# Kernel tuning notes

Hardware: AMD Instinct MI355X
Metric: run time of the kernel (lower is better)

The kernel has to match this reference:

```python
import jax, jax.numpy as jnp
from jax import lax
import numpy as np

W = 64          # net_width
NITER = 10
THRESH = 1e-3
MSTEP = 1.0


def setup_inputs() -> dict:
    key = jax.random.key(0)
    ks = jax.random.split(key, 10)
    B, Nh, DIM = 8, 16384, 1024
    eye = jnp.eye(W, dtype=jnp.float32)
    return {
        'y_re': jax.random.normal(ks[0], (B, 1, Nh), jnp.float32),
        'y_im': jax.random.normal(ks[1], (B, 1, Nh), jnp.float32),
        'H_re': jax.random.normal(ks[2], (32768, DIM), jnp.float32) / np.sqrt(DIM),
        'H_im': jax.random.normal(ks[3], (32768, DIM), jnp.float32) / np.sqrt(DIM),
        # torch inits: estep.weight=I, estep.bias=0, update.weight=I, memory.weight=1e-6*I;
        # add small perturbations so the math is non-degenerate.
        'estep_w': eye + 0.05 * jax.random.normal(ks[4], (W, W), jnp.float32),
        'estep_b': jnp.zeros((W,), jnp.float32),
        'update_w': eye + 0.05 * jax.random.normal(ks[5], (W, W), jnp.float32),
        'update_b': 0.02 * jax.random.normal(ks[6], (W,), jnp.float32),
        'memory_w': 1e-6 * eye + 0.01 * jax.random.normal(ks[7], (W, W), jnp.float32),
        'memory_b': 0.02 * jax.random.normal(ks[8], (W,), jnp.float32),
    }


def _forward(y_re, y_im, H_re, H_im, estep_w, estep_b, update_w, update_b, memory_w, memory_b):
    y = (y_re + 1j * y_im).astype(jnp.complex64)          # [B,1,Nh]
    y = jnp.concatenate([y, jnp.conj(y)], axis=2)         # [B,1,N]
    H = (H_re + 1j * H_im).astype(jnp.complex64)          # [N,DIM]
    B, N = y.shape[0], y.shape[2]
    DIM = H.shape[1]
    nb = N // W
    Hb = H.reshape(nb, W, DIM)                            # [nb,W,DIM]
    yb = y.reshape(B, nb, W).transpose(1, 0, 2)[:, :, None, :]  # [nb,B,1,W]

    x0 = jnp.zeros((B, 1, DIM), jnp.complex64)
    tau0 = jnp.ones((nb, B, 1, W), jnp.float32)

    def block_step(xk, blk):
        H_i, y_i, tau_i = blk                              # [W,DIM], [B,1,W], [B,1,W]
        zk = jnp.einsum('bod,wd->bow', xk, H_i)            # [B,1,W] complex
        r = y_i - zk
        a2 = jnp.abs(r) ** 2                               # [B,1,W] float32
        # expectation_step: xt / std(xt) (torch.std = unbiased, global)
        xt = a2 / jnp.std(a2, ddof=1)
        ht = jax.nn.sigmoid(xt @ estep_w.T + estep_b)
        tau_new = jax.nn.relu(ht @ update_w.T + update_b + tau_i @ memory_w.T + memory_b)
        sigma2 = jnp.mean(a2, axis=2, keepdims=True)       # [B,1,1]
        residual = MSTEP * r * tau_new / sigma2            # complex
        xk = xk + jnp.einsum('bow,wd->bod', residual, jnp.conj(H_i)) / (W * DIM)
        return xk, tau_new

    def iteration(carry, _):
        xk, tau = carry
        xk, tau_new = lax.scan(block_step, xk, (Hb, yb, tau))  # sequential over blocks
        # soft threshold: sgn(x) * relu(|x| - threshold * max|x|)
        ax = jnp.abs(xk)
        m = jnp.max(ax)
        sgn = jnp.where(ax > 0, xk / jnp.where(ax > 0, ax, 1.0), 0.0 + 0.0j)
        xk = sgn * jax.nn.relu(ax - THRESH * m)
        return (xk, tau_new), None

    (xk, tau), _ = lax.scan(iteration, (x0, tau0), None, length=NITER)
    tau_out = tau[:, :, 0, :].transpose(1, 0, 2)           # [B,nb,W]
    return jnp.real(xk), tau_out


def reference(y_re, y_im, H_re, H_im, estep_w, estep_b, update_w, update_b, memory_w, memory_b):
    return _forward(y_re, y_im, H_re, H_im, estep_w, estep_b,
                    update_w, update_b, memory_w, memory_b)
```

## Files before the change

### kernel.cpp

```cpp
#include <hip/hip_runtime.h>
#include <hip/hip_cooperative_groups.h>
#include <math.h>

namespace cg = cooperative_groups;

#define NT  256
#define NWG 64
#define SCOPE_AG __HIP_MEMORY_SCOPE_AGENT

__device__ __forceinline__ float ld_f(const float* p) {
    return __hip_atomic_load(p, __ATOMIC_RELAXED, SCOPE_AG);
}
__device__ __forceinline__ void st_f(float* p, float v) {
    __hip_atomic_store(p, v, __ATOMIC_RELAXED, SCOPE_AG);
}
__device__ __forceinline__ unsigned ld_u(const unsigned* p) {
    return __hip_atomic_load(p, __ATOMIC_RELAXED, SCOPE_AG);
}
__device__ __forceinline__ void st_u(unsigned* p, unsigned v) {
    __hip_atomic_store(p, v, __ATOMIC_RELAXED, SCOPE_AG);
}
__device__ __forceinline__ float2 ld_f2(const float2* p) {
    unsigned long long u = __hip_atomic_load((const unsigned long long*)p, __ATOMIC_RELAXED, SCOPE_AG);
    float2 r;
    r.x = __uint_as_float((unsigned)u);
    r.y = __uint_as_float((unsigned)(u >> 32));
    return r;
}
__device__ __forceinline__ void st_f2(float2* p, float2 v) {
    unsigned long long u = ((unsigned long long)__float_as_uint(v.y) << 32) | (unsigned long long)__float_as_uint(v.x);
    __hip_atomic_store((unsigned long long*)p, u, __ATOMIC_RELAXED, SCOPE_AG);
}

__device__ __forceinline__ float wsum64(float v) {
    #pragma unroll
    for (int m = 1; m < 64; m <<= 1) v += __shfl_xor(v, m);
    return v;
}
__device__ __forceinline__ float wmax64(float v) {
    #pragma unroll
    for (int m = 1; m < 64; m <<= 1) v = fmaxf(v, __shfl_xor(v, m));
    return v;
}


__launch_bounds__(NT, 1)
__global__ void robii_kernel(
    const float* __restrict__ y_re, const float* __restrict__ y_im,
    const float* __restrict__ H_re, const float* __restrict__ H_im,
    const float* __restrict__ estep_w, const float* __restrict__ estep_b,
    const float* __restrict__ update_w, const float* __restrict__ update_b,
    const float* __restrict__ memory_w, const float* __restrict__ memory_b,
    float* __restrict__ out, float* __restrict__ ws)
{
    cg::grid_group grid = cg::this_grid();

    __shared__ float wTe[4096], wTu[4096], wTm[4096];
    __shared__ float be[64], bu[64], bm[64];
    __shared__ float a2s[512];
    __shared__ float redl[8];
    __shared__ float gmax[1];
    __shared__ float2 rown[64];
    __shared__ float xts[64], hts[64], taurow[64];
    __shared__ float2 resid[64];
    __shared__ float2 cpartC[4][32][4];
    __shared__ float2 x_l[128];

    const int g = blockIdx.x, t = threadIdx.x;
    const int c = g & 7;
    const int b = g >> 3;
    const int lane = t & 63, wv = t >> 6;
    const int sub = t & 31;
    const int rbase = t >> 5;

    float2*   partws = (float2*)ws;
    float*    tauws  = ws + 16384;
    float*    pmws   = ws + 278528;
    unsigned* flags  = (unsigned*)(ws + 278592);

    for (int i = t; i < 4096; i += NT) {
        int j = i >> 6, k = i & 63;
        wTe[k * 64 + j] = estep_w[i];
        wTu[k * 64 + j] = update_w[i];
        wTm[k * 64 + j] = memory_w[i];
    }
    if (t < 64) { be[t] = estep_b[t]; bu[t] = update_b[t]; bm[t] = memory_b[t]; taurow[t] = 1.0f; }
    if (t < 128) x_l[t] = make_float2(0.0f, 0.0f);
    for (int i = t; i < 4096; i += NT) st_f(&tauws[g * 4096 + i], 1.0f);
    if (t == 0) st_u(&flags[g * 16], 0u);
    __threadfence();
    grid.sync();

    const size_t hcol = (size_t)c * 128 + (size_t)sub * 4;
    unsigned ep = 0;

    float4 hAre[8], hAim[8], hBre[8], hBim[8];

#define PREF(DRE, DIM_, BLKN) do {                                                   \
        const float* _pr = H_re + ((size_t)(BLKN) * 64 + rbase) * 1024 + hcol;       \
        const float* _pi = H_im + ((size_t)(BLKN) * 64 + rbase) * 1024 + hcol;       \
        _Pragma("unroll")                                                            \
        for (int _j = 0; _j < 8; ++_j) {                                             \
            DRE[_j]  = *(const float4*)(_pr + (size_t)_j * 8192);                    \
            DIM_[_j] = *(const float4*)(_pi + (size_t)_j * 8192);                    \
        }                                                                            \
    } while (0)

    PREF(hAre, hAim, 0);

#define STEP(BLK, CRE, CIM, NRE, NIM) do {                                           \
        const int blk = (BLK);                                                       \
        const int par = blk & 1;                                                     \
        __syncthreads();                               \
            \
        float2 xr0 = x_l[sub * 4 + 0], xr1 = x_l[sub * 4 + 1];                       \
        float2 xr2 = x_l[sub * 4 + 2], xr3 = x_l[sub * 4 + 3];                       \
        _Pragma("unroll")                                                            \
        for (int j = 0; j < 8; ++j) {                                                \
            float4 hr = CRE[j], hi = CIM[j];                                         \
            float sr, si;                                                            \
            sr  = xr0.x * hr.x - xr0.y * hi.x;  si  = xr0.x * hi.x + xr0.y * hr.x;   \
            sr += xr1.x * hr.y - xr1.y * hi.y;  si += xr1.x * hi.y + xr1.y * hr.y;   \
            sr += xr2.x * hr.z - xr2.y * hi.z;  si += xr2.x * hi.z + xr2.y * hr.z;   \
            sr += xr3.x * hr.w - xr3.y * hi.w;  si += xr3.x * hi.w + xr3.y * hr.w;   \
            _Pragma("unroll")                                                        \
            for (int m = 1; m < 32; m <<= 1) {                                       \
                sr += __shfl_xor(sr, m); si += __shfl_xor(si, m);                    \
            }                                                                        \
            if (sub == 0)                                                            \
                st_f2(&partws[par * 4096 + (b * 64 + rbase + 8 * j) * 8 + c],        \
                      make_float2(sr, si));                                          \
        }                                                                            \
        ++ep;                                                                        \
                       \
        __syncthreads();                                                             \
        if (t == 0) st_u(&flags[g * 16], ep);                                        \
          \
        PREF(NRE, NIM, ((blk + 1) & 511));                                           \
        float tau_nxt = 0.0f;                                                        \
        if (t < 64) tau_nxt = ld_f(&tauws[(((blk + 1) & 511) * 8 + b) * 64 + t]);    \
                           \
        if (t < 64) {                                                                \
            while (ld_u(&flags[t * 16]) < ep) __builtin_amdgcn_s_sleep(1);           \
        }                                                                            \
        __syncthreads();                                                             \
          \
        _Pragma("unroll")                                                            \
        for (int e = 0; e < 2; ++e) {                                                \
            int idx = t + e * 256;                                                   \
            int b1 = idx >> 6, w = idx & 63;                                         \
            const float2* pp = partws + (size_t)par * 4096 + (size_t)idx * 8;        \
            float zr = 0.0f, zi = 0.0f;                                              \
            _Pragma("unroll")                                                        \
            for (int cc = 0; cc < 8; ++cc) {                                         \
                float2 v = ld_f2(pp + cc);                                           \
                zr += v.x; zi += v.y;                                                \
            }                                                                        \
            int n = blk * 64 + w;                                                    \
            float yr, yi;                                                            \
            if (n < 16384) { yr = y_re[b1 * 16384 + n];         yi = y_im[b1 * 16384 + n]; } \
            else           { yr = y_re[b1 * 16384 + n - 16384]; yi = -y_im[b1 * 16384 + n - 16384]; } \
            float rr = yr - zr, ri = yi - zi;                                        \
            a2s[idx] = rr * rr + ri * ri;                                            \
            if (b1 == b) rown[w] = make_float2(rr, ri);                              \
        }                                                                            \
        __syncthreads();                                                             \
        float va = a2s[t] + a2s[t + 256];                                            \
        float s_ = wsum64(va);                                                       \
        if (lane == 0) redl[wv] = s_;                                                \
        __syncthreads();                                                             \
        float mean = (redl[0] + redl[1] + redl[2] + redl[3]) * (1.0f / 512.0f);      \
        float d0 = a2s[t] - mean, d1 = a2s[t + 256] - mean;                          \
        float s2_ = wsum64(d0 * d0 + d1 * d1);                                       \
        float sg  = wsum64(a2s[b * 64 + lane]) * (1.0f / 64.0f);                     \
        if (lane == 0) redl[4 + wv] = s2_;                                           \
        __syncthreads();                                                             \
        float stdv = sqrtf((redl[4] + redl[5] + redl[6] + redl[7]) * (1.0f / 511.0f)); \
        if (t < 64) xts[t] = a2s[b * 64 + t] / stdv;                                 \
        __syncthreads();                                                             \
        if (t < 64) {                                                                \
            float acc = be[t];                                                       \
            _Pragma("unroll")                                                        \
            for (int k = 0; k < 64; ++k) acc += wTe[k * 64 + t] * xts[k];            \
            hts[t] = 1.0f / (1.0f + expf(-acc));                                     \
        }                                                                            \
        __syncthreads();                                                             \
        if (t < 64) {                                                                \
            float acc = bu[t] + bm[t];                                               \
            _Pragma("unroll")                                                        \
            for (int k = 0; k < 64; ++k)                                             \
                acc += wTu[k * 64 + t] * hts[k] + wTm[k * 64 + t] * taurow[k];       \
            float tn = fmaxf(acc, 0.0f);                                             \
            if (c == 0) st_f(&tauws[(blk * 8 + b) * 64 + t], tn);                    \
            float2 rv = rown[t];                                                     \
            float scl = tn / sg;                                                     \
            resid[t] = make_float2(rv.x * scl, rv.y * scl);                          \
        }                                                                            \
        __syncthreads();                                                             \
            \
        float2 ac0 = make_float2(0.f, 0.f), ac1 = make_float2(0.f, 0.f);             \
        float2 ac2 = make_float2(0.f, 0.f), ac3 = make_float2(0.f, 0.f);             \
        _Pragma("unroll")                                                            \
        for (int j = 0; j < 8; ++j) {                                                \
            float2 rs = resid[rbase + 8 * j];                                        \
            float4 hr = CRE[j], hi = CIM[j];                                         \
            ac0.x += rs.x * hr.x + rs.y * hi.x;  ac0.y += rs.y * hr.x - rs.x * hi.x; \
            ac1.x += rs.x * hr.y + rs.y * hi.y;  ac1.y += rs.y * hr.y - rs.x * hi.y; \
            ac2.x += rs.x * hr.z + rs.y * hi.z;  ac2.y += rs.y * hr.z - rs.x * hi.z; \
            ac3.x += rs.x * hr.w + rs.y * hi.w;  ac3.y += rs.y * hr.w - rs.x * hi.w; \
        }                                                                            \
        ac0.x += __shfl_xor(ac0.x, 32); ac0.y += __shfl_xor(ac0.y, 32);              \
        ac1.x += __shfl_xor(ac1.x, 32); ac1.y += __shfl_xor(ac1.y, 32);              \
        ac2.x += __shfl_xor(ac2.x, 32); ac2.y += __shfl_xor(ac2.y, 32);              \
        ac3.x += __shfl_xor(ac3.x, 32); ac3.y += __shfl_xor(ac3.y, 32);              \
        if ((t & 32) == 0) {                                                         \
            cpartC[wv][sub][0] = ac0; cpartC[wv][sub][1] = ac1;                      \
            cpartC[wv][sub][2] = ac2; cpartC[wv][sub][3] = ac3;                      \
        }                                                                            \
        if (t < 64) taurow[t] = tau_nxt;                  \
        __syncthreads();                                                             \
        if (t < 128) {                                                               \
            int sl = t >> 2, kk = t & 3;                                             \
            float2 s0 = cpartC[0][sl][kk], s1 = cpartC[1][sl][kk];                   \
            float2 s2 = cpartC[2][sl][kk], s3 = cpartC[3][sl][kk];                   \
            float2 xv = x_l[t];                                                      \
            xv.x += (s0.x + s1.x + s2.x + s3.x) * (1.0f / 65536.0f);                 \
            xv.y += (s0.y + s1.y + s2.y + s3.y) * (1.0f / 65536.0f);                 \
            x_l[t] = xv;                                                             \
        }                                                                            \
    } while (0)

    #pragma unroll 1
    for (int iter = 0; iter < 10; ++iter) {
        #pragma unroll 1
        for (int blk2 = 0; blk2 < 512; blk2 += 2) {
            STEP(blk2,     hAre, hAim, hBre, hBim);
            STEP(blk2 + 1, hBre, hBim, hAre, hAim);
        }

        float lm = 0.0f;
        if (t < 128) { float2 xv = x_l[t]; lm = sqrtf(xv.x * xv.x + xv.y * xv.y); }
        lm = wmax64(lm);
        if (lane == 0) redl[wv] = lm;
        __syncthreads();
        if (t == 0) st_f(&pmws[g], fmaxf(fmaxf(redl[0], redl[1]), fmaxf(redl[2], redl[3])));
        ++ep;
        __syncthreads();
        if (t == 0) st_u(&flags[g * 16], ep);
        if (t < 64) {
            while (ld_u(&flags[t * 16]) < ep) __builtin_amdgcn_s_sleep(1);
        }
        __syncthreads();
        float pv = (t < 64) ? ld_f(&pmws[t]) : 0.0f;
        pv = wmax64(pv);
        if (t == 0) gmax[0] = pv;
        __syncthreads();
        float m = gmax[0];
        if (t < 128) {
            float2 xv = x_l[t];
            float ax = sqrtf(xv.x * xv.x + xv.y * xv.y);
            float s = (ax > 0.0f) ? fmaxf(ax - 1e-3f * m, 0.0f) / ax : 0.0f;
            x_l[t] = make_float2(xv.x * s, xv.y * s);
        }
        __syncthreads();
    }

    if (t < 128) out[b * 1024 + c * 128 + t] = x_l[t].x;
    for (int i = g * 8; i < g * 8 + 8; ++i) {
        for (int idx = t; idx < 512; idx += NT) {
            int bb = idx >> 6, w = idx & 63;
            out[8192 + bb * 32768 + i * 64 + w] = ld_f(&tauws[(i * 8 + bb) * 64 + w]);
        }
    }
#undef STEP
#undef PREF
}

extern "C" void kernel_launch(void* const* d_in, const int* in_sizes, int n_in,
                              void* d_out, int out_size, void* d_ws, size_t ws_size,
                              hipStream_t stream) {
    (void)in_sizes; (void)n_in; (void)out_size; (void)ws_size;
    const float* y_re     = (const float*)d_in[0];
    const float* y_im     = (const float*)d_in[1];
    const float* H_re     = (const float*)d_in[2];
    const float* H_im     = (const float*)d_in[3];
    const float* estep_w  = (const float*)d_in[4];
    const float* estep_b  = (const float*)d_in[5];
    const float* update_w = (const float*)d_in[6];
    const float* update_b = (const float*)d_in[7];
    const float* memory_w = (const float*)d_in[8];
    const float* memory_b = (const float*)d_in[9];
    float* outp = (float*)d_out;
    float* wsp  = (float*)d_ws;

    void* args[] = {
        (void*)&y_re, (void*)&y_im, (void*)&H_re, (void*)&H_im,
        (void*)&estep_w, (void*)&estep_b, (void*)&update_w, (void*)&update_b,
        (void*)&memory_w, (void*)&memory_b, (void*)&outp, (void*)&wsp
    };
    hipLaunchCooperativeKernel((void*)robii_kernel, dim3(NWG), dim3(NT), args, 0, stream);
}
```

Measured before the change: 42.31 ms.

## Replace cooperative launch with parity-plane flag barriers and parallelize small matvecs

Drops the cooperative-groups launch and grid.sync in favour of a plain launch. Cross-workgroup barriers now use flag slots alternating between two parity planes with equality checks. The y loads are moved ahead of the spin-wait so they overlap barrier latency. The two 64x64 matvecs (estep, and update+memory) are split across all 256 threads with a shared-memory partial reduction, instead of running serially on 64 threads. A diagnostic kernel writes sentinel values if the launch fails. The risk is that co-residency of all 64 workgroups is no longer guaranteed by the runtime, and stale flag values from an earlier call could in principle interfere.

```diff
diff --git a/kernel.cpp b/kernel.cpp
--- a/kernel.cpp
+++ b/kernel.cpp
@@ -1,8 +1,5 @@
 #include <hip/hip_runtime.h>
-#include <hip/hip_cooperative_groups.h>
 #include <math.h>
-
-namespace cg = cooperative_groups;
 
 #define NT  256
 #define NWG 64
@@ -53,8 +50,6 @@
     const float* __restrict__ memory_w, const float* __restrict__ memory_b,
     float* __restrict__ out, float* __restrict__ ws)
 {
-    cg::grid_group grid = cg::this_grid();
-
     __shared__ float wTe[4096], wTu[4096], wTm[4096];
     __shared__ float be[64], bu[64], bm[64];
     __shared__ float a2s[512];
@@ -66,6 +61,8 @@
     __shared__ float2 cpartC[4][32][4];
     __shared__ float2 x_l[128];
 
+    float* mpartf = (float*)cpartC;
+
     const int g = blockIdx.x, t = threadIdx.x;
     const int c = g & 7;
     const int b = g >> 3;
@@ -87,12 +84,19 @@
     if (t < 64) { be[t] = estep_b[t]; bu[t] = update_b[t]; bm[t] = memory_b[t]; taurow[t] = 1.0f; }
     if (t < 128) x_l[t] = make_float2(0.0f, 0.0f);
     for (int i = t; i < 4096; i += NT) st_f(&tauws[g * 4096 + i], 1.0f);
-    if (t == 0) st_u(&flags[g * 16], 0u);
-    __threadfence();
-    grid.sync();
+
+    unsigned ep = 1;
+    {
+        unsigned* plane = flags + ((ep & 1u) << 9);
+        __syncthreads();
+        if (t == 0) st_u(&plane[g * 8], ep);
+        if (t < 64) {
+            while (ld_u(&plane[t * 8]) != ep) __builtin_amdgcn_s_sleep(1);
+        }
+        __syncthreads();
+    }
 
     const size_t hcol = (size_t)c * 128 + (size_t)sub * 4;
-    unsigned ep = 0;
 
     float4 hAre[8], hAim[8], hBre[8], hBim[8];
 
@@ -132,19 +136,30 @@
                       make_float2(sr, si));                                          \
         }                                                                            \
         ++ep;                                                                        \
+        unsigned* plane = flags + ((ep & 1u) << 9);                                  \
                        \
         __syncthreads();                                                             \
-        if (t == 0) st_u(&flags[g * 16], ep);                                        \
-          \
+        if (t == 0) st_u(&plane[g * 8], ep);                                         \
+                \
         PREF(NRE, NIM, ((blk + 1) & 511));                                           \
         float tau_nxt = 0.0f;                                                        \
         if (t < 64) tau_nxt = ld_f(&tauws[(((blk + 1) & 511) * 8 + b) * 64 + t]);    \
-                           \
+        float yAr, yAi, yBr, yBi;                                                    \
+        {                                                                            \
+            int b1 = t >> 6, w1 = t & 63, n1 = blk * 64 + w1;                        \
+            if (n1 < 16384) { yAr = y_re[b1 * 16384 + n1];         yAi = y_im[b1 * 16384 + n1]; } \
+            else            { yAr = y_re[b1 * 16384 + n1 - 16384]; yAi = -y_im[b1 * 16384 + n1 - 16384]; } \
+            int i2 = t + 256;                                                        \
+            int b2 = i2 >> 6, w2 = i2 & 63, n2 = blk * 64 + w2;                      \
+            if (n2 < 16384) { yBr = y_re[b2 * 16384 + n2];         yBi = y_im[b2 * 16384 + n2]; } \
+            else            { yBr = y_re[b2 * 16384 + n2 - 16384]; yBi = -y_im[b2 * 16384 + n2 - 16384]; } \
+        }                                                                            \
+                \
         if (t < 64) {                                                                \
-            while (ld_u(&flags[t * 16]) < ep) __builtin_amdgcn_s_sleep(1);           \
-        }                                                                            \
-        __syncthreads();                                                             \
-          \
+            while (ld_u(&plane[t * 8]) != ep) __builtin_amdgcn_s_sleep(1);           \
+        }                                                                            \
+        __syncthreads();                                                             \
+                                      \
         _Pragma("unroll")                                                            \
         for (int e = 0; e < 2; ++e) {                                                \
             int idx = t + e * 256;                                                   \
@@ -156,15 +171,13 @@
                 float2 v = ld_f2(pp + cc);                                           \
                 zr += v.x; zi += v.y;                                                \
             }                                                                        \
-            int n = blk * 64 + w;                                                    \
-            float yr, yi;                                                            \
-            if (n < 16384) { yr = y_re[b1 * 16384 + n];         yi = y_im[b1 * 16384 + n]; } \
-            else           { yr = y_re[b1 * 16384 + n - 16384]; yi = -y_im[b1 * 16384 + n - 16384]; } \
-            float rr = yr - zr, ri = yi - zi;                                        \
+            float rr = ((e == 0) ? yAr : yBr) - zr;                                  \
+            float ri = ((e == 0) ? yAi : yBi) - zi;                                  \
             a2s[idx] = rr * rr + ri * ri;                                            \
             if (b1 == b) rown[w] = make_float2(rr, ri);                              \
         }                                                                            \
         __syncthreads();                                                             \
+                                       \
         float va = a2s[t] + a2s[t + 256];                                            \
         float s_ = wsum64(va);                                                       \
         if (lane == 0) redl[wv] = s_;                                                \
@@ -178,19 +191,38 @@
         float stdv = sqrtf((redl[4] + redl[5] + redl[6] + redl[7]) * (1.0f / 511.0f)); \
         if (t < 64) xts[t] = a2s[b * 64 + t] / stdv;                                 \
         __syncthreads();                                                             \
+          \
+        {                                                                            \
+            int j = t & 63, q = t >> 6;                                              \
+            float acc = 0.0f;                                                        \
+            _Pragma("unroll")                                                        \
+            for (int k16 = 0; k16 < 16; ++k16) {                                     \
+                int k = q * 16 + k16;                                                \
+                acc += wTe[k * 64 + j] * xts[k];                                     \
+            }                                                                        \
+            mpartf[q * 64 + j] = acc;                                                \
+        }                                                                            \
+        __syncthreads();                                                             \
         if (t < 64) {                                                                \
-            float acc = be[t];                                                       \
+            float acc = be[t] + mpartf[t] + mpartf[64 + t] + mpartf[128 + t] + mpartf[192 + t]; \
+            hts[t] = 1.0f / (1.0f + expf(-acc));                                     \
+        }                                                                            \
+        __syncthreads();                                                             \
+                          \
+        {                                                                            \
+            int j = t & 63, q = t >> 6;                                              \
+            float acc = 0.0f;                                                        \
             _Pragma("unroll")                                                        \
-            for (int k = 0; k < 64; ++k) acc += wTe[k * 64 + t] * xts[k];            \
-            hts[t] = 1.0f / (1.0f + expf(-acc));                                     \
+            for (int k16 = 0; k16 < 16; ++k16) {                                     \
+                int k = q * 16 + k16;                                                \
+                acc += wTu[k * 64 + j] * hts[k] + wTm[k * 64 + j] * taurow[k];       \
+            }                                                                        \
+            mpartf[q * 64 + j] = acc;                                                \
         }                                                                            \
         __syncthreads();                                                             \
         if (t < 64) {                                                                \
-            float acc = bu[t] + bm[t];                                               \
-            _Pragma("unroll")                                                        \
-            for (int k = 0; k < 64; ++k)                                             \
-                acc += wTu[k * 64 + t] * hts[k] + wTm[k * 64 + t] * taurow[k];       \
-            float tn = fmaxf(acc, 0.0f);                                             \
+            float tn = bu[t] + bm[t] + mpartf[t] + mpartf[64 + t] + mpartf[128 + t] + mpartf[192 + t]; \
+            tn = fmaxf(tn, 0.0f);                                                    \
             if (c == 0) st_f(&tauws[(blk * 8 + b) * 64 + t], tn);                    \
             float2 rv = rown[t];                                                     \
             float scl = tn / sg;                                                     \
@@ -245,12 +277,15 @@
         __syncthreads();
         if (t == 0) st_f(&pmws[g], fmaxf(fmaxf(redl[0], redl[1]), fmaxf(redl[2], redl[3])));
         ++ep;
-        __syncthreads();
-        if (t == 0) st_u(&flags[g * 16], ep);
-        if (t < 64) {
-            while (ld_u(&flags[t * 16]) < ep) __builtin_amdgcn_s_sleep(1);
-        }
-        __syncthreads();
+        {
+            unsigned* plane = flags + ((ep & 1u) << 9);
+            __syncthreads();
+            if (t == 0) st_u(&plane[g * 8], ep);
+            if (t < 64) {
+                while (ld_u(&plane[t * 8]) != ep) __builtin_amdgcn_s_sleep(1);
+            }
+            __syncthreads();
+        }
         float pv = (t < 64) ? ld_f(&pmws[t]) : 0.0f;
         pv = wmax64(pv);
         if (t == 0) gmax[0] = pv;
@@ -274,6 +309,11 @@
     }
 #undef STEP
 #undef PREF
+}
+
+__global__ void robii_diag_kernel(float* out, int code) {
+    int i = blockIdx.x * blockDim.x + threadIdx.x;
+    if (i < 8192) out[i] = 1.0e6f * (float)(1 + code);
 }
 
 extern "C" void kernel_launch(void* const* d_in, const int* in_sizes, int n_in,
@@ -293,10 +333,12 @@
     float* outp = (float*)d_out;
     float* wsp  = (float*)d_ws;
 
-    void* args[] = {
-        (void*)&y_re, (void*)&y_im, (void*)&H_re, (void*)&H_im,
-        (void*)&estep_w, (void*)&estep_b, (void*)&update_w, (void*)&update_b,
-        (void*)&memory_w, (void*)&memory_b, (void*)&outp, (void*)&wsp
-    };
-    hipLaunchCooperativeKernel((void*)robii_kernel, dim3(NWG), dim3(NT), args, 0, stream);
-}
+    hipLaunchKernelGGL(robii_kernel, dim3(NWG), dim3(NT), 0, stream,
+                       y_re, y_im, H_re, H_im, estep_w, estep_b,
+                       update_w, update_b, memory_w, memory_b, outp, wsp);
+    hipError_t e = hipGetLastError();
+    if (e != hipSuccess) {
+        hipLaunchKernelGGL(robii_diag_kernel, dim3(32), dim3(256), 0, stream,
+                           outp, (int)e);
+    }
+}
```

New measurement: 39.18 ms. -7.4%, faster.
